# Optimization experiments

Measured on AMD Instinct MI355X. Metric: run time of the kernel, lower is better.

Reference implementation:

```python
import jax, jax.numpy as jnp
import numpy as np

DIM, NH, HD = 1536, 12, 128
C = HD // 2            # 64 complex (half) dims per head
BANDS = (C - 2 * (C // 3), C // 3, C // 3)   # (22, 21, 21) for T/H/W
EPS = 1e-6
F, Hg, Wg = 6, 20, 32
S = F * Hg * Wg
MAX_LEN = 1024


def _rope_tables(max_len=MAX_LEN):
    # Wan-style 1D rope params per band, concatenated along channel dim -> [max_len, 64]
    pos = np.arange(max_len, dtype=np.float64)
    cos_l, sin_l = [], []
    for bd in BANDS:
        inv = 1.0 / (10000.0 ** (np.arange(bd, dtype=np.float64) / bd))
        ang = np.outer(pos, inv)
        cos_l.append(np.cos(ang))
        sin_l.append(np.sin(ang))
    return (np.concatenate(cos_l, 1).astype(np.float32),
            np.concatenate(sin_l, 1).astype(np.float32))


def setup_inputs() -> dict:
    key = jax.random.key(0)
    ks = jax.random.split(key, 8)
    std = 0.02
    fc, fs = _rope_tables()
    return {
        "x": jax.random.normal(ks[0], (1, S, DIM), jnp.float32),
        "Wq": jax.random.normal(ks[1], (DIM, DIM), jnp.float32) * std,
        "bq": jnp.zeros((DIM,), jnp.float32),
        "Wk": jax.random.normal(ks[2], (DIM, DIM), jnp.float32) * std,
        "bk": jnp.zeros((DIM,), jnp.float32),
        "Wv": jax.random.normal(ks[3], (DIM, DIM), jnp.float32) * std,
        "bv": jnp.zeros((DIM,), jnp.float32),
        "Wo": jax.random.normal(ks[4], (DIM, DIM), jnp.float32) * std,
        "bo": jnp.zeros((DIM,), jnp.float32),
        "gq": jnp.ones((DIM,), jnp.float32),
        "gk": jnp.ones((DIM,), jnp.float32),
        "freqs_cos": jnp.asarray(fc),
        "freqs_sin": jnp.asarray(fs),
        "f": F, "h": Hg, "w": Wg,
    }


def _rmsnorm(t, g):
    t = t.astype(jnp.float32)
    return t * jax.lax.rsqrt(jnp.mean(t * t, axis=-1, keepdims=True) + EPS) * g


def _grid_freqs(tab, f, h, w):
    # tab: [max_len, 64] -> [f*h*w, 64] via T/H/W band broadcast (mirrors torch expand+cat)
    o1, o2 = BANDS[0], BANDS[0] + BANDS[1]
    t = jnp.broadcast_to(tab[:f, None, None, :o1], (f, h, w, BANDS[0]))
    hh = jnp.broadcast_to(tab[None, :h, None, o1:o2], (f, h, w, BANDS[1]))
    ww = jnp.broadcast_to(tab[None, None, :w, o2:C], (f, h, w, BANDS[2]))
    return jnp.concatenate([t, hh, ww], axis=-1).reshape(f * h * w, 1, C)


def _rope_apply(t, fc, fs):
    # t: [B, S, n, d]; complex mul (a+ib)*(cos+isin) on pairs of channels
    B, Sl, n, d = t.shape
    tr = t.astype(jnp.float32).reshape(B, Sl, n, C, 2)
    a, b = tr[..., 0], tr[..., 1]
    fc = fc[None]  # [1, S, 1, C]
    fs = fs[None]
    out_r = a * fc - b * fs
    out_i = a * fs + b * fc
    return jnp.stack([out_r, out_i], axis=-1).reshape(B, Sl, n, d)


def reference(x, Wq, bq, Wk, bk, Wv, bv, Wo, bo, gq, gk, freqs_cos, freqs_sin, f, h, w):
    B, Sl, _ = x.shape
    q = _rmsnorm(x @ Wq.T + bq, gq).reshape(B, Sl, NH, HD)
    k = _rmsnorm(x @ Wk.T + bk, gk).reshape(B, Sl, NH, HD)
    v = (x @ Wv.T + bv).reshape(B, Sl, NH, HD)

    fc = _grid_freqs(freqs_cos, f, h, w)
    fs = _grid_freqs(freqs_sin, f, h, w)
    q = _rope_apply(q, fc, fs)
    k = _rope_apply(k, fc, fs)

    scale = 1.0 / jnp.sqrt(jnp.float32(HD))
    scores = jnp.einsum('bqnd,bknd->bnqk', q, k) * scale
    p = jax.nn.softmax(scores, axis=-1)
    o = jnp.einsum('bnqk,bknd->bqnd', p, v.astype(jnp.float32))
    o = o.reshape(B, Sl, DIM)
    return o @ Wo.T + bo
```

## Files before the change

kernel.cpp:

```cpp
#include <hip/hip_runtime.h>
#include <hip/hip_bf16.h>
#include <cstdint>

#define DIM 1536
#define NHEADS 12
#define HD 128
#define SEQ 3840
#define SCL2F 0.1275365308119098f
#define THRRAW 90.50966799187809f

typedef float f32x4 __attribute__((ext_vector_type(4)));
typedef __bf16 bf16x8 __attribute__((ext_vector_type(8)));
typedef __bf16 bf16x4 __attribute__((ext_vector_type(4)));
typedef __bf16 bf16x2 __attribute__((ext_vector_type(2)));
typedef unsigned int u32;
typedef u32 u32x4 __attribute__((ext_vector_type(4)));

#define GLLD(g, l) __builtin_amdgcn_global_load_lds( \
    (const __attribute__((address_space(1))) void*)(g), \
    (__attribute__((address_space(3))) void*)(l), 16, 0, 0)

__global__ __launch_bounds__(256) void cvt_bf16_5(
    const float* __restrict__ s0, const float* __restrict__ s1, const float* __restrict__ s2,
    const float* __restrict__ s3, const float* __restrict__ s4,
    __bf16* __restrict__ d0, __bf16* __restrict__ d1, __bf16* __restrict__ d2,
    __bf16* __restrict__ d3, __bf16* __restrict__ d4,
    int n4_0, int n4_w) {
    const float* src; __bf16* dst; int n4;
    switch (blockIdx.y) {
        case 0: src = s0; dst = d0; n4 = n4_0; break;
        case 1: src = s1; dst = d1; n4 = n4_w; break;
        case 2: src = s2; dst = d2; n4 = n4_w; break;
        case 3: src = s3; dst = d3; n4 = n4_w; break;
        default: src = s4; dst = d4; n4 = n4_w; break;
    }
    int i = blockIdx.x * 256 + threadIdx.x;
    if (i < n4) {
        f32x4 v = ((const f32x4*)src)[i];
        bf16x4 o;
        o[0] = (__bf16)v[0]; o[1] = (__bf16)v[1];
        o[2] = (__bf16)v[2]; o[3] = (__bf16)v[3];
        ((bf16x4*)dst)[i] = o;
    }
}

template <int OUTF32>
__global__ __launch_bounds__(256, 2) void gemm256(
    const __bf16* __restrict__ A,
    const __bf16* __restrict__ B0, const __bf16* __restrict__ B1, const __bf16* __restrict__ B2,
    const float* __restrict__ bias0, const float* __restrict__ bias1, const float* __restrict__ bias2,
    void* __restrict__ C0v, void* __restrict__ C1v, void* __restrict__ C2v,
    int N, int K) {
    const __bf16* B = B0; const float* bias = bias0; void* Cv = C0v;
    if (blockIdx.z == 1) { B = B1; bias = bias1; Cv = C1v; }
    else if (blockIdx.z == 2) { B = B2; bias = bias2; Cv = C2v; }

    __shared__ __bf16 sA[3][256 * 32];
    __shared__ __bf16 sB[3][128 * 32];

    const int t = threadIdx.x;
    const int wid = t >> 6, lane = t & 63;
    const int lr = lane & 15, lg = lane >> 4;
    const int wr = (wid >> 1) * 128, wc = (wid & 1) * 64;

    const __bf16* pa = A + ((long long)blockIdx.y * 256 + (t >> 2)) * K + (t & 3) * 8;
    const __bf16* pb = B + ((long long)blockIdx.x * 128 + (t >> 2)) * K + (t & 3) * 8;
    const int ldsbase = wid * 512;

    auto stage = [&](int kk, int bufi) {
#pragma unroll
        for (int r = 0; r < 4; r++)
            GLLD(pa + (long long)(r * 64) * K + kk, &sA[bufi][r * 2048 + ldsbase]);
#pragma unroll
        for (int r = 0; r < 2; r++)
            GLLD(pb + (long long)(r * 64) * K + kk, &sB[bufi][r * 2048 + ldsbase]);
    };

    f32x4 acc[8][4] = {};
    const int NT = K / 32;

    stage(0, 0);
    stage(32, 1);
    asm volatile("s_waitcnt vmcnt(6)" ::: "memory");
    __builtin_amdgcn_s_barrier();
    __builtin_amdgcn_sched_barrier(0);

    int c0 = 0, c2 = 2;
#pragma unroll 1
    for (int i = 0; i < NT; i++) {
        const __bf16* sAc = &sA[0][0] + c0 * (256 * 32);
        const __bf16* sBc = &sB[0][0] + c0 * (128 * 32);
        bf16x8 af[8], bfr[4];
#pragma unroll
        for (int mI = 0; mI < 8; mI++)
            af[mI] = *(const bf16x8*)(sAc + (wr + mI * 16 + lr) * 32 + lg * 8);
#pragma unroll
        for (int nI = 0; nI < 4; nI++)
            bfr[nI] = *(const bf16x8*)(sBc + (wc + nI * 16 + lr) * 32 + lg * 8);
        if (i + 2 < NT) stage((i + 2) * 32, c2);

        __builtin_amdgcn_s_setprio(1);
#pragma unroll
        for (int mI = 0; mI < 8; mI++) {
            acc[mI][0] = __builtin_amdgcn_mfma_f32_16x16x32_bf16(af[mI], bfr[0], acc[mI][0], 0, 0, 0);
            acc[mI][1] = __builtin_amdgcn_mfma_f32_16x16x32_bf16(af[mI], bfr[1], acc[mI][1], 0, 0, 0);
        }
        __builtin_amdgcn_s_setprio(0);
        __builtin_amdgcn_s_barrier();
        __builtin_amdgcn_s_setprio(1);
#pragma unroll
        for (int mI = 0; mI < 8; mI++) {
            acc[mI][2] = __builtin_amdgcn_mfma_f32_16x16x32_bf16(af[mI], bfr[2], acc[mI][2], 0, 0, 0);
            acc[mI][3] = __builtin_amdgcn_mfma_f32_16x16x32_bf16(af[mI], bfr[3], acc[mI][3], 0, 0, 0);
        }
        __builtin_amdgcn_s_setprio(0);

        if (i + 2 < NT) asm volatile("s_waitcnt vmcnt(6)" ::: "memory");
        else            asm volatile("s_waitcnt vmcnt(0)" ::: "memory");
        __builtin_amdgcn_s_barrier();
        __builtin_amdgcn_sched_barrier(0);
        c0 = (c0 == 2) ? 0 : c0 + 1;
        c2 = (c2 == 2) ? 0 : c2 + 1;
    }

    const int cb = blockIdx.x * 128 + wc;
    const int rb_ = blockIdx.y * 256 + wr;
#pragma unroll
    for (int nI = 0; nI < 4; nI++) {
        int col = cb + nI * 16 + lr;
        float bv = bias[col];
#pragma unroll
        for (int mI = 0; mI < 8; mI++) {
            int row0 = rb_ + mI * 16 + lg * 4;
#pragma unroll
            for (int r = 0; r < 4; r++) {
                float v = acc[mI][nI][r] + bv;
                if (OUTF32) ((float*)Cv)[(long long)(row0 + r) * N + col] = v;
                else ((__bf16*)Cv)[(long long)(row0 + r) * N + col] = (__bf16)v;
            }
        }
    }
}

__global__ __launch_bounds__(256) void norm_rope2(
    const __bf16* __restrict__ qpre, const __bf16* __restrict__ kpre,
    const float* __restrict__ gq, const float* __restrict__ gk,
    const float* __restrict__ fcos, const float* __restrict__ fsin,
    __bf16* __restrict__ Qb, __bf16* __restrict__ Kb) {
    const __bf16* pre = blockIdx.y ? kpre : qpre;
    const float* gvec = blockIdx.y ? gk : gq;
    __bf16* out = blockIdx.y ? Kb : Qb;
    const int s = blockIdx.x;
    const int t = threadIdx.x;
    float a[3], b[3];
    float ss = 0.f;
#pragma unroll
    for (int j = 0; j < 3; j++) {
        int p = t + 256 * j;
        bf16x2 v = *(const bf16x2*)(pre + (size_t)s * DIM + 2 * p);
        a[j] = (float)v[0]; b[j] = (float)v[1];
        ss += a[j] * a[j] + b[j] * b[j];
    }
    for (int off = 32; off; off >>= 1) ss += __shfl_down(ss, off);
    __shared__ float red[4];
    if ((t & 63) == 0) red[t >> 6] = ss;
    __syncthreads();
    float mean = (red[0] + red[1] + red[2] + red[3]) * (1.f / DIM);
    float rms = rsqrtf(mean + 1e-6f);
    const int fi = s / 640, hi2 = (s % 640) >> 5, wi = s & 31;
#pragma unroll
    for (int j = 0; j < 3; j++) {
        int p = t + 256 * j;
        int c = p & 63;
        int pos = (c < 22) ? fi : ((c < 43) ? hi2 : wi);
        float fc = fcos[pos * 64 + c];
        float fs = fsin[pos * 64 + c];
        float av = a[j] * rms * gvec[2 * p];
        float bv = b[j] * rms * gvec[2 * p + 1];
        float orr = av * fc - bv * fs;
        float oi = av * fs + bv * fc;
        int hh = p >> 6;
        bf16x2 o; o[0] = (__bf16)orr; o[1] = (__bf16)oi;
        *(bf16x2*)(out + ((size_t)hh * SEQ + s) * HD + 2 * c) = o;
    }
}

__global__ __launch_bounds__(256) void transpose_bf16(
    const __bf16* __restrict__ in, __bf16* __restrict__ out) {
    __shared__ __bf16 tile[64][68];
    const int t = threadIdx.x;
    const int sb = blockIdx.x * 64, cb = blockIdx.y * 64;
    const int tx = t & 15, ty = t >> 4;
#pragma unroll
    for (int i = 0; i < 4; i++) {
        int r = ty + i * 16;
        bf16x4 v = *(const bf16x4*)(in + (size_t)(sb + r) * DIM + cb + tx * 4);
        *(bf16x4*)&tile[r][tx * 4] = v;
    }
    __syncthreads();
    int s0 = sb + tx * 4;
    int j = (s0 >> 2) & 7;
    int u = (j < 4) ? (j << 1) : ((j << 1) - 7);
    int sp = (s0 & ~31) + (u << 2);
#pragma unroll
    for (int i = 0; i < 4; i++) {
        int c = ty + i * 16;
        bf16x4 v;
        v[0] = tile[tx * 4 + 0][c]; v[1] = tile[tx * 4 + 1][c];
        v[2] = tile[tx * 4 + 2][c]; v[3] = tile[tx * 4 + 3][c];
        *(bf16x4*)(out + (size_t)(cb + c) * SEQ + sp) = v;
    }
}

__global__ __launch_bounds__(256, 4) void attn_split(
    const __bf16* __restrict__ Q, const __bf16* __restrict__ Kk,
    const __bf16* __restrict__ Vp,
    float* __restrict__ pacc,
    float2* __restrict__ pml) {
    __shared__ __bf16 Ks[2][32 * 128];
    __shared__ __bf16 Vs[2][128 * 32];
    const int bid = blockIdx.x;
    const int task = (bid & 7) * 180 + (bid >> 3);
    const int half = task & 1;
    const int hq = task >> 1;
    const int h = hq / 60;
    const int qb = hq % 60;
    const int t = threadIdx.x;
    const int wv = t >> 6;
    const int lane = t & 63;
    const int lq = lane & 15, g = lane >> 4;
    const int q0 = qb * 64 + wv * 16;
    const int kvbase = half * (SEQ / 2);
    const __bf16* Qh = Q + (size_t)h * SEQ * HD;
    const __bf16* Kh = Kk + (size_t)h * SEQ * HD;
    const __bf16* Vh = Vp + (size_t)h * HD * SEQ;

    bf16x8 qf[4];
#pragma unroll
    for (int c = 0; c < 4; c++)
        qf[c] = *(const bf16x8*)(Qh + (size_t)(q0 + lq) * HD + c * 32 + g * 8);

    f32x4 acc[8] = {};
    float m = -1e30f;
    float lp = 0.f;

    const int krow_in = lane >> 4;
    const int vrow_in = lane >> 2;
    const int vce = (lane & 3) * 8;
    auto stage = [&](int kv0, int b) {
#pragma unroll
        for (int c = wv; c < 16; c += 4) {
            if (c < 8) {
                int r = c * 4 + krow_in;
                int cb = ((lane & 15) * 16) ^ ((r & 7) << 4);
                GLLD(Kh + (size_t)(kv0 + r) * HD + (cb >> 1), &Ks[b][c * 512]);
            } else {
                int cc = c - 8;
                int rd = cc * 16 + vrow_in;
                GLLD(Vh + (size_t)rd * SEQ + kv0 + vce, &Vs[b][cc * 512]);
            }
        }
    };

    stage(kvbase, 0);
    int buf = 0;
    const int kswz = (lq & 7) << 3;
#pragma unroll 1
    for (int i = 0; i < 60; i++) {
        __syncthreads();
        if (i + 1 < 60) stage(kvbase + (i + 1) * 32, buf ^ 1);
        const __bf16* Kb_ = &Ks[buf][0];
        const __bf16* Vb_ = &Vs[buf][0];

        f32x4 sc0 = {0.f, 0.f, 0.f, 0.f}, sc1 = {0.f, 0.f, 0.f, 0.f};
        __builtin_amdgcn_s_setprio(1);
#pragma unroll
        for (int c = 0; c < 4; c++) {
            int cb = (c * 32 + g * 8) ^ kswz;
            bf16x8 k0 = *(const bf16x8*)(Kb_ + lq * 128 + cb);
            bf16x8 k1 = *(const bf16x8*)(Kb_ + (16 + lq) * 128 + cb);
            sc0 = __builtin_amdgcn_mfma_f32_16x16x32_bf16(k0, qf[c], sc0, 0, 0, 0);
            sc1 = __builtin_amdgcn_mfma_f32_16x16x32_bf16(k1, qf[c], sc1, 0, 0, 0);
        }
        __builtin_amdgcn_s_setprio(0);

        bf16x8 vf[8];
#pragma unroll
        for (int dt = 0; dt < 8; dt++)
            vf[dt] = *(const bf16x8*)(Vb_ + (dt * 16 + lq) * 32 + g * 8);

        float pm = fmaxf(fmaxf(fmaxf(sc0[0], sc0[1]), fmaxf(sc0[2], sc0[3])),
                         fmaxf(fmaxf(sc1[0], sc1[1]), fmaxf(sc1[2], sc1[3])));
        if (!__all(pm <= m + THRRAW)) {
            pm = fmaxf(pm, __shfl_xor(pm, 16));
            pm = fmaxf(pm, __shfl_xor(pm, 32));
            float mn = fmaxf(m, pm);
            float al = __builtin_amdgcn_exp2f(SCL2F * (m - mn));
            m = mn; lp *= al;
#pragma unroll
            for (int dt = 0; dt < 8; dt++)
#pragma unroll
                for (int r = 0; r < 4; r++) acc[dt][r] *= al;
        }
        float ms = SCL2F * m;
        float p[8], ls = 0.f;
#pragma unroll
        for (int r = 0; r < 4; r++) { p[r] = __builtin_amdgcn_exp2f(SCL2F * sc0[r] - ms); ls += p[r]; }
#pragma unroll
        for (int r = 0; r < 4; r++) { p[4 + r] = __builtin_amdgcn_exp2f(SCL2F * sc1[r] - ms); ls += p[4 + r]; }
        lp += ls;
        bf16x8 pa;
#pragma unroll
        for (int i2 = 0; i2 < 8; i2++) pa[i2] = (__bf16)p[i2];

        __builtin_amdgcn_s_setprio(1);
#pragma unroll
        for (int dt = 0; dt < 8; dt++)
            acc[dt] = __builtin_amdgcn_mfma_f32_16x16x32_bf16(vf[dt], pa, acc[dt], 0, 0, 0);
        __builtin_amdgcn_s_setprio(0);
        buf ^= 1;
    }

    float lps = lp;
    lps += __shfl_xor(lps, 16);
    lps += __shfl_xor(lps, 32);
    const size_t qrow = (size_t)(half * NHEADS + h) * SEQ + q0 + lq;
    if (g == 0) pml[qrow] = float2{m, lps};
#pragma unroll
    for (int dt = 0; dt < 8; dt++)
        *(f32x4*)(pacc + qrow * HD + dt * 16 + g * 4) = acc[dt];
}

__global__ __launch_bounds__(256) void attn_merge(
    const float* __restrict__ pacc, const float2* __restrict__ pml,
    __bf16* __restrict__ ob) {
    const int t = threadIdx.x;
    const int qq = blockIdx.x * 8 + (t >> 5);
    const int d = (t & 31) * 4;
    float2 a = pml[qq], b = pml[NHEADS * SEQ + qq];
    float M = fmaxf(a.x, b.x);
    float w0 = __builtin_amdgcn_exp2f(SCL2F * (a.x - M));
    float w1 = __builtin_amdgcn_exp2f(SCL2F * (b.x - M));
    float den = 1.f / (a.y * w0 + b.y * w1);
    f32x4 n0 = *(const f32x4*)(pacc + (size_t)qq * HD + d);
    f32x4 n1 = *(const f32x4*)(pacc + ((size_t)NHEADS * SEQ + qq) * HD + d);
    int h = qq / SEQ, s = qq % SEQ;
    bf16x4 o;
#pragma unroll
    for (int r = 0; r < 4; r++) o[r] = (__bf16)((n0[r] * w0 + n1[r] * w1) * den);
    *(bf16x4*)(ob + (size_t)s * DIM + h * HD + d) = o;
}

__global__ __launch_bounds__(256, 4) void attn_single(
    const __bf16* __restrict__ Q, const __bf16* __restrict__ Kk,
    const __bf16* __restrict__ Vp, __bf16* __restrict__ O) {
    __shared__ __bf16 Ks[2][32 * 128];
    __shared__ __bf16 Vs[2][128 * 32];
    const int bid = blockIdx.x;
    const int task = (bid & 7) * 90 + (bid >> 3);
    const int h = task / 60;
    const int qb = task % 60;
    const int t = threadIdx.x;
    const int wv = t >> 6;
    const int lane = t & 63;
    const int lq = lane & 15, g = lane >> 4;
    const int q0 = qb * 64 + wv * 16;
    const __bf16* Qh = Q + (size_t)h * SEQ * HD;
    const __bf16* Kh = Kk + (size_t)h * SEQ * HD;
    const __bf16* Vh = Vp + (size_t)h * HD * SEQ;
    bf16x8 qf[4];
#pragma unroll
    for (int c = 0; c < 4; c++)
        qf[c] = *(const bf16x8*)(Qh + (size_t)(q0 + lq) * HD + c * 32 + g * 8);
    f32x4 acc[8] = {};
    float m = -1e30f, lp = 0.f;
    const int krow_in = lane >> 4;
    const int vrow_in = lane >> 2;
    const int vce = (lane & 3) * 8;
    auto stage = [&](int kv0, int b) {
#pragma unroll
        for (int c = wv; c < 16; c += 4) {
            if (c < 8) {
                int r = c * 4 + krow_in;
                int cb = ((lane & 15) * 16) ^ ((r & 7) << 4);
                GLLD(Kh + (size_t)(kv0 + r) * HD + (cb >> 1), &Ks[b][c * 512]);
            } else {
                int cc = c - 8;
                int rd = cc * 16 + vrow_in;
                GLLD(Vh + (size_t)rd * SEQ + kv0 + vce, &Vs[b][cc * 512]);
            }
        }
    };
    stage(0, 0);
    int buf = 0;
    const int kswz = (lq & 7) << 3;
#pragma unroll 1
    for (int i = 0; i < 120; i++) {
        __syncthreads();
        if (i + 1 < 120) stage((i + 1) * 32, buf ^ 1);
        const __bf16* Kb_ = &Ks[buf][0];
        const __bf16* Vb_ = &Vs[buf][0];
        f32x4 sc0 = {0.f, 0.f, 0.f, 0.f}, sc1 = {0.f, 0.f, 0.f, 0.f};
#pragma unroll
        for (int c = 0; c < 4; c++) {
            int cb = (c * 32 + g * 8) ^ kswz;
            bf16x8 k0 = *(const bf16x8*)(Kb_ + lq * 128 + cb);
            bf16x8 k1 = *(const bf16x8*)(Kb_ + (16 + lq) * 128 + cb);
            sc0 = __builtin_amdgcn_mfma_f32_16x16x32_bf16(k0, qf[c], sc0, 0, 0, 0);
            sc1 = __builtin_amdgcn_mfma_f32_16x16x32_bf16(k1, qf[c], sc1, 0, 0, 0);
        }
        bf16x8 vf[8];
#pragma unroll
        for (int dt = 0; dt < 8; dt++)
            vf[dt] = *(const bf16x8*)(Vb_ + (dt * 16 + lq) * 32 + g * 8);
        float pm = fmaxf(fmaxf(fmaxf(sc0[0], sc0[1]), fmaxf(sc0[2], sc0[3])),
                         fmaxf(fmaxf(sc1[0], sc1[1]), fmaxf(sc1[2], sc1[3])));
        if (!__all(pm <= m + THRRAW)) {
            pm = fmaxf(pm, __shfl_xor(pm, 16));
            pm = fmaxf(pm, __shfl_xor(pm, 32));
            float mn = fmaxf(m, pm);
            float al = __builtin_amdgcn_exp2f(SCL2F * (m - mn));
            m = mn; lp *= al;
#pragma unroll
            for (int dt = 0; dt < 8; dt++)
#pragma unroll
                for (int r = 0; r < 4; r++) acc[dt][r] *= al;
        }
        float ms = SCL2F * m;
        float p[8], ls = 0.f;
#pragma unroll
        for (int r = 0; r < 4; r++) { p[r] = __builtin_amdgcn_exp2f(SCL2F * sc0[r] - ms); ls += p[r]; }
#pragma unroll
        for (int r = 0; r < 4; r++) { p[4 + r] = __builtin_amdgcn_exp2f(SCL2F * sc1[r] - ms); ls += p[4 + r]; }
        lp += ls;
        bf16x8 pa;
#pragma unroll
        for (int i2 = 0; i2 < 8; i2++) pa[i2] = (__bf16)p[i2];
#pragma unroll
        for (int dt = 0; dt < 8; dt++)
            acc[dt] = __builtin_amdgcn_mfma_f32_16x16x32_bf16(vf[dt], pa, acc[dt], 0, 0, 0);
        buf ^= 1;
    }
    float lps = lp;
    lps += __shfl_xor(lps, 16);
    lps += __shfl_xor(lps, 32);
    float inv = 1.f / lps;
#pragma unroll
    for (int dt = 0; dt < 8; dt++) {
        bf16x4 o;
#pragma unroll
        for (int r = 0; r < 4; r++) o[r] = (__bf16)(acc[dt][r] * inv);
        *(bf16x4*)(O + (size_t)(q0 + lq) * DIM + h * HD + dt * 16 + g * 4) = o;
    }
}

extern "C" void kernel_launch(void* const* d_in, const int* in_sizes, int n_in,
                              void* d_out, int out_size, void* d_ws, size_t ws_size,
                              hipStream_t stream) {
    const float* x = (const float*)d_in[0];
    const float* Wq = (const float*)d_in[1];
    const float* bq = (const float*)d_in[2];
    const float* Wk = (const float*)d_in[3];
    const float* bk = (const float*)d_in[4];
    const float* Wv = (const float*)d_in[5];
    const float* bv = (const float*)d_in[6];
    const float* Wo = (const float*)d_in[7];
    const float* bo = (const float*)d_in[8];
    const float* gq = (const float*)d_in[9];
    const float* gk = (const float*)d_in[10];
    const float* fcos = (const float*)d_in[11];
    const float* fsin = (const float*)d_in[12];
    float* out = (float*)d_out;

    char* p = (char*)d_ws;
    const size_t SZ_SD = (size_t)SEQ * DIM * 2;
    const size_t SZ_W = (size_t)DIM * DIM * 2;
    __bf16* xb   = (__bf16*)p;  p += SZ_SD;
    __bf16* Wob  = (__bf16*)p;  p += SZ_W;
    __bf16* Wqb  = (__bf16*)p;  p += SZ_W;
    __bf16* Wkb  = (__bf16*)p;  p += SZ_W;
    __bf16* Wvb  = (__bf16*)p;  p += SZ_W;
    __bf16* qpre = (__bf16*)p;  p += SZ_SD;
    __bf16* kpre = (__bf16*)p;  p += SZ_SD;
    __bf16* vpre = (__bf16*)p;  p += SZ_SD;
    __bf16* Kb   = (__bf16*)p;  p += SZ_SD;
    __bf16* Vtb  = (__bf16*)p;  p += SZ_SD;
    float2* pml  = (float2*)p;  p += sizeof(float2) * 2 * NHEADS * SEQ;
    float* pacc = (float*)Wqb;
    __bf16* Qb = xb;
    const bool split_ok = ws_size >= (size_t)(p - (char*)d_ws);

    const int n4_x = SEQ * DIM / 4;
    const int n4_w = DIM * DIM / 4;
    cvt_bf16_5<<<dim3((n4_x + 255) / 256, 5), 256, 0, stream>>>(
        x, Wq, Wk, Wv, Wo, xb, Wqb, Wkb, Wvb, Wob, n4_x, n4_w);

    gemm256<0><<<dim3(DIM / 128, SEQ / 256, 3), 256, 0, stream>>>(
        xb, Wqb, Wkb, Wvb, bq, bk, bv, qpre, kpre, vpre, DIM, DIM);

    norm_rope2<<<dim3(SEQ, 2), 256, 0, stream>>>(qpre, kpre, gq, gk, fcos, fsin, Qb, Kb);
    transpose_bf16<<<dim3(SEQ / 64, DIM / 64), 256, 0, stream>>>(vpre, Vtb);

    if (split_ok) {
        __bf16* ob = Kb;
        attn_split<<<dim3(1440), 256, 0, stream>>>(Qb, Kb, Vtb, pacc, pml);
        attn_merge<<<dim3(NHEADS * SEQ / 8), 256, 0, stream>>>(pacc, pml, ob);
        gemm256<1><<<dim3(DIM / 128, SEQ / 256, 1), 256, 0, stream>>>(
            ob, Wob, Wob, Wob, bo, bo, bo, out, out, out, DIM, DIM);
    } else {
        __bf16* ob = qpre;
        attn_single<<<dim3(720), 256, 0, stream>>>(Qb, Kb, Vtb, ob);
        gemm256<1><<<dim3(DIM / 128, SEQ / 256, 1), 256, 0, stream>>>(
            ob, Wob, Wob, Wob, bo, bo, bo, out, out, out, DIM, DIM);
    }
}
```

Before: 296.0 us.

## Process two query groups per wave in split attention to reuse K/V tiles

Each wave in the split attention kernel now handles 32 query rows (two 16-row groups) instead of 16, so each block covers 128 queries. Every K and V fragment read from LDS feeds twice as many MFMAs, and each block stages K/V tiles for twice the work, halving global-to-LDS traffic per query. The grid drops from 1440 to 720 blocks, and occupancy bounds are relaxed to 3 blocks per SM to leave room for the doubled accumulator registers. Staging address math is also precomputed outside the loop. The trade-off is higher register pressure and fewer blocks to spread across the CUs.

```diff
diff --git a/kernel.cpp b/kernel.cpp
--- a/kernel.cpp
+++ b/kernel.cpp
@@ -212,7 +212,7 @@
     }
 }
 
-__global__ __launch_bounds__(256, 4) void attn_split(
+__global__ __launch_bounds__(256, 3) void attn_split(
     const __bf16* __restrict__ Q, const __bf16* __restrict__ Kk,
     const __bf16* __restrict__ Vp,
     float* __restrict__ pacc,
@@ -220,67 +220,66 @@
     __shared__ __bf16 Ks[2][32 * 128];
     __shared__ __bf16 Vs[2][128 * 32];
     const int bid = blockIdx.x;
-    const int task = (bid & 7) * 180 + (bid >> 3);
+    const int task = (bid & 7) * 90 + (bid >> 3);
     const int half = task & 1;
     const int hq = task >> 1;
-    const int h = hq / 60;
-    const int qb = hq % 60;
+    const int h = hq / 30;
+    const int qb = hq % 30;
     const int t = threadIdx.x;
     const int wv = t >> 6;
     const int lane = t & 63;
     const int lq = lane & 15, g = lane >> 4;
-    const int q0 = qb * 64 + wv * 16;
+    const int q0 = qb * 128 + wv * 32;
     const int kvbase = half * (SEQ / 2);
     const __bf16* Qh = Q + (size_t)h * SEQ * HD;
     const __bf16* Kh = Kk + (size_t)h * SEQ * HD;
     const __bf16* Vh = Vp + (size_t)h * HD * SEQ;
 
-    bf16x8 qf[4];
-#pragma unroll
-    for (int c = 0; c < 4; c++)
-        qf[c] = *(const bf16x8*)(Qh + (size_t)(q0 + lq) * HD + c * 32 + g * 8);
-
-    f32x4 acc[8] = {};
-    float m = -1e30f;
-    float lp = 0.f;
-
-    const int krow_in = lane >> 4;
-    const int vrow_in = lane >> 2;
-    const int vce = (lane & 3) * 8;
-    auto stage = [&](int kv0, int b) {
-#pragma unroll
-        for (int c = wv; c < 16; c += 4) {
-            if (c < 8) {
-                int r = c * 4 + krow_in;
-                int cb = ((lane & 15) * 16) ^ ((r & 7) << 4);
-                GLLD(Kh + (size_t)(kv0 + r) * HD + (cb >> 1), &Ks[b][c * 512]);
-            } else {
-                int cc = c - 8;
-                int rd = cc * 16 + vrow_in;
-                GLLD(Vh + (size_t)rd * SEQ + kv0 + vce, &Vs[b][cc * 512]);
-            }
-        }
+    bf16x8 qf[2][4];
+#pragma unroll
+    for (int qg = 0; qg < 2; qg++)
+#pragma unroll
+        for (int c = 0; c < 4; c++)
+            qf[qg][c] = *(const bf16x8*)(Qh + (size_t)(q0 + qg * 16 + lq) * HD + c * 32 + g * 8);
+
+    f32x4 acc[8][2] = {};
+    float m[2] = {-1e30f, -1e30f};
+    float lp[2] = {0.f, 0.f};
+
+    const int krow0 = wv * 4 + (lane >> 4);
+    const int kcb = ((lane & 15) * 16) ^ ((krow0 & 7) << 4);
+    const __bf16* kp = Kh + (size_t)(kvbase + krow0) * HD + (kcb >> 1);
+    const __bf16* vp = Vh + (size_t)(wv * 16 + (lane >> 2)) * SEQ + kvbase + (lane & 3) * 8;
+    auto stage = [&](int i, int b) {
+        const __bf16* kpi = kp + (size_t)i * 32 * HD;
+        const __bf16* vpi = vp + i * 32;
+        GLLD(kpi,           &Ks[b][wv * 512]);
+        GLLD(kpi + 16 * HD, &Ks[b][(wv + 4) * 512]);
+        GLLD(vpi,            &Vs[b][wv * 512]);
+        GLLD(vpi + 64 * SEQ, &Vs[b][(wv + 4) * 512]);
     };
 
-    stage(kvbase, 0);
+    stage(0, 0);
     int buf = 0;
     const int kswz = (lq & 7) << 3;
 #pragma unroll 1
     for (int i = 0; i < 60; i++) {
         __syncthreads();
-        if (i + 1 < 60) stage(kvbase + (i + 1) * 32, buf ^ 1);
+        if (i + 1 < 60) stage(i + 1, buf ^ 1);
         const __bf16* Kb_ = &Ks[buf][0];
         const __bf16* Vb_ = &Vs[buf][0];
 
-        f32x4 sc0 = {0.f, 0.f, 0.f, 0.f}, sc1 = {0.f, 0.f, 0.f, 0.f};
+        f32x4 sc[2][2] = {};
         __builtin_amdgcn_s_setprio(1);
 #pragma unroll
         for (int c = 0; c < 4; c++) {
             int cb = (c * 32 + g * 8) ^ kswz;
             bf16x8 k0 = *(const bf16x8*)(Kb_ + lq * 128 + cb);
             bf16x8 k1 = *(const bf16x8*)(Kb_ + (16 + lq) * 128 + cb);
-            sc0 = __builtin_amdgcn_mfma_f32_16x16x32_bf16(k0, qf[c], sc0, 0, 0, 0);
-            sc1 = __builtin_amdgcn_mfma_f32_16x16x32_bf16(k1, qf[c], sc1, 0, 0, 0);
+            sc[0][0] = __builtin_amdgcn_mfma_f32_16x16x32_bf16(k0, qf[0][c], sc[0][0], 0, 0, 0);
+            sc[0][1] = __builtin_amdgcn_mfma_f32_16x16x32_bf16(k0, qf[1][c], sc[0][1], 0, 0, 0);
+            sc[1][0] = __builtin_amdgcn_mfma_f32_16x16x32_bf16(k1, qf[0][c], sc[1][0], 0, 0, 0);
+            sc[1][1] = __builtin_amdgcn_mfma_f32_16x16x32_bf16(k1, qf[1][c], sc[1][1], 0, 0, 0);
         }
         __builtin_amdgcn_s_setprio(0);
 
@@ -289,46 +288,54 @@
         for (int dt = 0; dt < 8; dt++)
             vf[dt] = *(const bf16x8*)(Vb_ + (dt * 16 + lq) * 32 + g * 8);
 
-        float pm = fmaxf(fmaxf(fmaxf(sc0[0], sc0[1]), fmaxf(sc0[2], sc0[3])),
-                         fmaxf(fmaxf(sc1[0], sc1[1]), fmaxf(sc1[2], sc1[3])));
-        if (!__all(pm <= m + THRRAW)) {
-            pm = fmaxf(pm, __shfl_xor(pm, 16));
-            pm = fmaxf(pm, __shfl_xor(pm, 32));
-            float mn = fmaxf(m, pm);
-            float al = __builtin_amdgcn_exp2f(SCL2F * (m - mn));
-            m = mn; lp *= al;
-#pragma unroll
-            for (int dt = 0; dt < 8; dt++)
-#pragma unroll
-                for (int r = 0; r < 4; r++) acc[dt][r] *= al;
-        }
-        float ms = SCL2F * m;
-        float p[8], ls = 0.f;
-#pragma unroll
-        for (int r = 0; r < 4; r++) { p[r] = __builtin_amdgcn_exp2f(SCL2F * sc0[r] - ms); ls += p[r]; }
-#pragma unroll
-        for (int r = 0; r < 4; r++) { p[4 + r] = __builtin_amdgcn_exp2f(SCL2F * sc1[r] - ms); ls += p[4 + r]; }
-        lp += ls;
-        bf16x8 pa;
-#pragma unroll
-        for (int i2 = 0; i2 < 8; i2++) pa[i2] = (__bf16)p[i2];
+        bf16x8 pa[2];
+#pragma unroll
+        for (int qg = 0; qg < 2; qg++) {
+            float pm = fmaxf(fmaxf(fmaxf(sc[0][qg][0], sc[0][qg][1]), fmaxf(sc[0][qg][2], sc[0][qg][3])),
+                             fmaxf(fmaxf(sc[1][qg][0], sc[1][qg][1]), fmaxf(sc[1][qg][2], sc[1][qg][3])));
+            if (!__all(pm <= m[qg] + THRRAW)) {
+                pm = fmaxf(pm, __shfl_xor(pm, 16));
+                pm = fmaxf(pm, __shfl_xor(pm, 32));
+                float mn = fmaxf(m[qg], pm);
+                float al = __builtin_amdgcn_exp2f(SCL2F * (m[qg] - mn));
+                m[qg] = mn; lp[qg] *= al;
+#pragma unroll
+                for (int dt = 0; dt < 8; dt++)
+#pragma unroll
+                    for (int r = 0; r < 4; r++) acc[dt][qg][r] *= al;
+            }
+            float ms = SCL2F * m[qg];
+            float p[8], ls = 0.f;
+#pragma unroll
+            for (int r = 0; r < 4; r++) { p[r] = __builtin_amdgcn_exp2f(SCL2F * sc[0][qg][r] - ms); ls += p[r]; }
+#pragma unroll
+            for (int r = 0; r < 4; r++) { p[4 + r] = __builtin_amdgcn_exp2f(SCL2F * sc[1][qg][r] - ms); ls += p[4 + r]; }
+            lp[qg] += ls;
+#pragma unroll
+            for (int i2 = 0; i2 < 8; i2++) pa[qg][i2] = (__bf16)p[i2];
+        }
 
         __builtin_amdgcn_s_setprio(1);
 #pragma unroll
-        for (int dt = 0; dt < 8; dt++)
-            acc[dt] = __builtin_amdgcn_mfma_f32_16x16x32_bf16(vf[dt], pa, acc[dt], 0, 0, 0);
+        for (int dt = 0; dt < 8; dt++) {
+            acc[dt][0] = __builtin_amdgcn_mfma_f32_16x16x32_bf16(vf[dt], pa[0], acc[dt][0], 0, 0, 0);
+            acc[dt][1] = __builtin_amdgcn_mfma_f32_16x16x32_bf16(vf[dt], pa[1], acc[dt][1], 0, 0, 0);
+        }
         __builtin_amdgcn_s_setprio(0);
         buf ^= 1;
     }
 
-    float lps = lp;
-    lps += __shfl_xor(lps, 16);
-    lps += __shfl_xor(lps, 32);
-    const size_t qrow = (size_t)(half * NHEADS + h) * SEQ + q0 + lq;
-    if (g == 0) pml[qrow] = float2{m, lps};
-#pragma unroll
-    for (int dt = 0; dt < 8; dt++)
-        *(f32x4*)(pacc + qrow * HD + dt * 16 + g * 4) = acc[dt];
+#pragma unroll
+    for (int qg = 0; qg < 2; qg++) {
+        float lps = lp[qg];
+        lps += __shfl_xor(lps, 16);
+        lps += __shfl_xor(lps, 32);
+        const size_t qrow = (size_t)(half * NHEADS + h) * SEQ + q0 + qg * 16 + lq;
+        if (g == 0) pml[qrow] = float2{m[qg], lps};
+#pragma unroll
+        for (int dt = 0; dt < 8; dt++)
+            *(f32x4*)(pacc + qrow * HD + dt * 16 + g * 4) = acc[dt][qg];
+    }
 }
 
 __global__ __launch_bounds__(256) void attn_merge(
@@ -503,7 +510,7 @@
 
     if (split_ok) {
         __bf16* ob = Kb;
-        attn_split<<<dim3(1440), 256, 0, stream>>>(Qb, Kb, Vtb, pacc, pml);
+        attn_split<<<dim3(720), 256, 0, stream>>>(Qb, Kb, Vtb, pacc, pml);
         attn_merge<<<dim3(NHEADS * SEQ / 8), 256, 0, stream>>>(pacc, pml, ob);
         gemm256<1><<<dim3(DIM / 128, SEQ / 256, 1), 256, 0, stream>>>(
             ob, Wob, Wob, Wob, bo, bo, bo, out, out, out, DIM, DIM);
```

New measurement: 271.9 us. 8.1% less time.
